# Kernel optimization log

Measured on AMD Instinct MI355X. Metric: run time of the kernel, lower is better.

The kernel has to match this reference:

```python
import jax, jax.numpy as jnp
import numpy as np

N, C, NS = 131072, 128, 16
BN_EPS = 1e-5


def setup_inputs() -> dict:
    key = jax.random.key(0)
    ks = jax.random.split(key, 8)
    p = jax.random.normal(ks[0], (N, 3), dtype=jnp.float32)
    u = jax.random.normal(ks[1], (N, C), dtype=jnp.float32)
    o = jnp.array([N], dtype=jnp.int32)  # batch offset (single cloud)
    idx = jax.random.randint(ks[2], (N, NS), 0, N, dtype=jnp.int32)  # precomputed KNN indices
    s = 1.0 / np.sqrt(C)
    W1 = jax.random.uniform(ks[3], (C, C), jnp.float32, -s, s)
    b1 = jax.random.uniform(ks[4], (C,), jnp.float32, -s, s)
    W2 = jax.random.uniform(ks[5], (C, C), jnp.float32, -s, s)
    b2 = jax.random.uniform(ks[6], (C,), jnp.float32, -s, s)
    gamma = jnp.ones((C,), jnp.float32)
    beta = jnp.zeros((C,), jnp.float32)
    return {"p": p, "u": u, "o": o, "idx": idx, "W1": W1, "b1": b1,
            "W2": W2, "b2": b2, "gamma": gamma, "beta": beta}


def reference(p, u, o, idx, W1, b1, W2, b2, gamma, beta):
    # pre_trans: Linear(d_in, d_in)
    u_pre = u @ W1 + b1                                  # [N, C]
    # queryandgroup (use_xyz=False): gather neighbor features by KNN idx
    u_n = u_pre[idx]                                     # [N, NS, C] irregular gather
    # local Laplacian: ReLU(neighbor - center), mean over neighborhood
    lap = jnp.maximum(u_n - u_pre[:, None, :], 0.0).mean(axis=1)  # [N, C]
    # varphi: Linear -> BatchNorm1d (training stats) -> ReLU
    h = lap @ W2 + b2                                    # [N, C]
    mean = h.mean(axis=0)
    var = ((h - mean) ** 2).mean(axis=0)  # biased var, as BN normalization uses
    h = (h - mean) * jax.lax.rsqrt(var + BN_EPS) * gamma + beta
    u_tt = jnp.maximum(h, 0.0)
    return (p, u_tt, o)
```

## Files before the change

### kernel.cpp

```cpp
#include <hip/hip_runtime.h>

#define N_PTS 131072
#define C_DIM 128
#define NS_K  16
#define BN_EPS 1e-5f

typedef unsigned short ushort_t;
typedef unsigned short u16x8 __attribute__((ext_vector_type(8)));
typedef __bf16 bf16x8 __attribute__((ext_vector_type(8)));
typedef float f32x4 __attribute__((ext_vector_type(4)));

__device__ __forceinline__ ushort_t f2b(float f) {
    unsigned int u = __float_as_uint(f);
    u += 0x7FFFu + ((u >> 16) & 1u);
    return (ushort_t)(u >> 16);
}
__device__ __forceinline__ float b2f(ushort_t h) {
    return __uint_as_float((unsigned int)h << 16);
}

__global__ __launch_bounds__(256) void prep_w_kernel(
    const float* __restrict__ W1, const float* __restrict__ W2,
    ushort_t* __restrict__ wT1, ushort_t* __restrict__ wT2)
{
    const int t = blockIdx.x * 256 + threadIdx.x;
    const int n = t & 127;
    const int k = t >> 7;
    wT1[n * 128 + k] = f2b(W1[k * 128 + n]);
    wT2[n * 128 + k] = f2b(W2[k * 128 + n]);
}

template <bool A_BF16, bool STATS>
__global__ __launch_bounds__(256) void gemm_mfma_kernel(
    const void* __restrict__ Aptr, const ushort_t* __restrict__ wT,
    const float* __restrict__ bias, ushort_t* __restrict__ out,
    float* __restrict__ gsum, float* __restrict__ gsq)
{
    __shared__ __align__(16) ushort_t a_sh[128 * 136];
    __shared__ __align__(16) ushort_t w_sh[128 * 136];
    __shared__ float s_sum[128];
    __shared__ float s_sq[128];

    const int tid  = threadIdx.x;
    const int lane = tid & 63;
    const int wv   = tid >> 6;
    const int m16  = lane & 15;
    const int q    = lane >> 4;
    const int base = blockIdx.x * 128;

    if (STATS && tid < 128) { s_sum[tid] = 0.f; s_sq[tid] = 0.f; }

    {
        const int row  = tid >> 1;
        const int half = (tid & 1) * 64;
        ushort_t* as = a_sh + row * 136 + half;
        if (A_BF16) {
            const ushort_t* ag = (const ushort_t*)Aptr + (size_t)(base + row) * 128 + half;
            #pragma unroll
            for (int j = 0; j < 8; j++)
                *(u16x8*)(as + j * 8) = *(const u16x8*)(ag + j * 8);
        } else {
            const float* ag = (const float*)Aptr + (size_t)(base + row) * 128 + half;
            #pragma unroll
            for (int j = 0; j < 8; j++) {
                f32x4 lo = *(const f32x4*)(ag + j * 8);
                f32x4 hi = *(const f32x4*)(ag + j * 8 + 4);
                u16x8 v;
                v[0] = f2b(lo[0]); v[1] = f2b(lo[1]); v[2] = f2b(lo[2]); v[3] = f2b(lo[3]);
                v[4] = f2b(hi[0]); v[5] = f2b(hi[1]); v[6] = f2b(hi[2]); v[7] = f2b(hi[3]);
                *(u16x8*)(as + j * 8) = v;
            }
        }
    }
    {
        const int n    = tid >> 1;
        const int half = (tid & 1) * 64;
        const ushort_t* wg = wT + (size_t)n * 128 + half;
        ushort_t* ws = w_sh + n * 136 + half;
        #pragma unroll
        for (int j = 0; j < 8; j++)
            *(u16x8*)(ws + j * 8) = *(const u16x8*)(wg + j * 8);
    }
    __syncthreads();

    f32x4 acc[2][8];
    #pragma unroll
    for (int i = 0; i < 2; i++)
        #pragma unroll
        for (int c = 0; c < 8; c++) acc[i][c] = (f32x4){0.f, 0.f, 0.f, 0.f};

    const ushort_t* ap0 = a_sh + ((wv * 2 + 0) * 16 + m16) * 136 + q * 8;
    const ushort_t* ap1 = a_sh + ((wv * 2 + 1) * 16 + m16) * 136 + q * 8;
    const ushort_t* wp  = w_sh + m16 * 136 + q * 8;

    #pragma unroll
    for (int k0 = 0; k0 < 128; k0 += 32) {
        bf16x8 a0 = __builtin_bit_cast(bf16x8, *(const u16x8*)(ap0 + k0));
        bf16x8 a1 = __builtin_bit_cast(bf16x8, *(const u16x8*)(ap1 + k0));
        #pragma unroll
        for (int c = 0; c < 8; c++) {
            bf16x8 b = __builtin_bit_cast(bf16x8, *(const u16x8*)(wp + c * (16 * 136) + k0));
            acc[0][c] = __builtin_amdgcn_mfma_f32_16x16x32_bf16(a0, b, acc[0][c], 0, 0, 0);
            acc[1][c] = __builtin_amdgcn_mfma_f32_16x16x32_bf16(a1, b, acc[1][c], 0, 0, 0);
        }
    }

    __syncthreads();

    float psum[8], psq[8];
    #pragma unroll
    for (int c = 0; c < 8; c++) { psum[c] = 0.f; psq[c] = 0.f; }

    #pragma unroll
    for (int c = 0; c < 8; c++) {
        const int col = c * 16 + m16;
        const float bv = bias[col];
        #pragma unroll
        for (int i = 0; i < 2; i++) {
            const int rb = (wv * 2 + i) * 16 + q * 4;
            #pragma unroll
            for (int r = 0; r < 4; r++) {
                const float v = acc[i][c][r] + bv;
                a_sh[(rb + r) * 136 + col] = f2b(v);
                if (STATS) { psum[c] += v; psq[c] += v * v; }
            }
        }
    }
    if (STATS) {
        #pragma unroll
        for (int c = 0; c < 8; c++) {
            atomicAdd(&s_sum[c * 16 + m16], psum[c]);
            atomicAdd(&s_sq[c * 16 + m16],  psq[c]);
        }
    }
    __syncthreads();

    {
        const int r0 = tid >> 4;
        const int c0 = (tid & 15) * 8;
        #pragma unroll
        for (int it = 0; it < 8; it++) {
            const int rl = r0 + it * 16;
            const u16x8 v = *(const u16x8*)(a_sh + rl * 136 + c0);
            *(u16x8*)(out + (size_t)(base + rl) * 128 + c0) = v;
        }
    }
    if (STATS && tid < 128) {
        atomicAdd(&gsum[tid], s_sum[tid]);
        atomicAdd(&gsq[tid],  s_sq[tid]);
    }
}

__global__ __launch_bounds__(256) void laplacian_kernel(
    const ushort_t* __restrict__ table, const int* __restrict__ idx,
    ushort_t* __restrict__ lap)
{
    __shared__ int s_idx[256];
    const int tid = threadIdx.x;
    s_idx[tid] = idx[blockIdx.x * 256 + tid];
    __syncthreads();

    const int p  = tid >> 4;
    const int c8 = (tid & 15) * 8;
    const size_t pt = (size_t)blockIdx.x * 16 + p;

    const u16x8 cv = *(const u16x8*)(table + pt * 128 + c8);
    float ctr[8];
    #pragma unroll
    for (int e = 0; e < 8; e++) ctr[e] = b2f(cv[e]);

    float acc[8];
    #pragma unroll
    for (int e = 0; e < 8; e++) acc[e] = 0.f;

    #pragma unroll
    for (int s = 0; s < NS_K; s++) {
        const int j = s_idx[p * 16 + s];
        const u16x8 nv = *(const u16x8*)(table + (size_t)j * 128 + c8);
        #pragma unroll
        for (int e = 0; e < 8; e++)
            acc[e] += fmaxf(b2f(nv[e]) - ctr[e], 0.f);
    }

    u16x8 o;
    #pragma unroll
    for (int e = 0; e < 8; e++) o[e] = f2b(acc[e] * (1.f / (float)NS_K));
    *(u16x8*)(lap + pt * 128 + c8) = o;
}

__global__ void bn_stats_kernel(const float* __restrict__ gsum,
                                const float* __restrict__ gsq,
                                const float* __restrict__ gamma,
                                const float* __restrict__ beta,
                                float* __restrict__ bnsc, float* __restrict__ bnsh)
{
    const int c = threadIdx.x;
    const float invN = 1.f / (float)N_PTS;
    const float mean = gsum[c] * invN;
    const float var  = gsq[c] * invN - mean * mean;
    const float sc   = rsqrtf(var + BN_EPS) * gamma[c];
    bnsc[c] = sc;
    bnsh[c] = fmaf(-mean, sc, beta[c]);
}

__global__ __launch_bounds__(256) void bn_relu_kernel(
    const ushort_t* __restrict__ h, const float* __restrict__ bnsc,
    const float* __restrict__ bnsh, float* __restrict__ out)
{
    const size_t i = (size_t)blockIdx.x * 256 + threadIdx.x;
    const int c8 = (threadIdx.x * 8) & 127;

    const u16x8 hv = *(const u16x8*)(h + i * 8);
    const f32x4 sc0 = *(const f32x4*)(bnsc + c8);
    const f32x4 sc1 = *(const f32x4*)(bnsc + c8 + 4);
    const f32x4 sh0 = *(const f32x4*)(bnsh + c8);
    const f32x4 sh1 = *(const f32x4*)(bnsh + c8 + 4);

    f32x4 o0, o1;
    #pragma unroll
    for (int e = 0; e < 4; e++) {
        o0[e] = fmaxf(fmaf(b2f(hv[e]),     sc0[e], sh0[e]), 0.f);
        o1[e] = fmaxf(fmaf(b2f(hv[4 + e]), sc1[e], sh1[e]), 0.f);
    }
    float* op = out + (size_t)3 * N_PTS + i * 8;
    *(f32x4*)(op)     = o0;
    *(f32x4*)(op + 4) = o1;
}

__global__ __launch_bounds__(256) void copy_p_kernel(
    const float* __restrict__ p, const int* __restrict__ o,
    float* __restrict__ out)
{
    const size_t i = (size_t)blockIdx.x * 256 + threadIdx.x;
    *(f32x4*)(out + i * 4) = *(const f32x4*)(p + i * 4);
    if (i == 0)
        out[(size_t)3 * N_PTS + (size_t)N_PTS * C_DIM] = (float)o[0];
}

extern "C" void kernel_launch(void* const* d_in, const int* in_sizes, int n_in,
                              void* d_out, int out_size, void* d_ws, size_t ws_size,
                              hipStream_t stream) {
    const float* p     = (const float*)d_in[0];
    const float* u     = (const float*)d_in[1];
    const int*   o     = (const int*)d_in[2];
    const int*   idx   = (const int*)d_in[3];
    const float* W1    = (const float*)d_in[4];
    const float* b1    = (const float*)d_in[5];
    const float* W2    = (const float*)d_in[6];
    const float* b2    = (const float*)d_in[7];
    const float* gamma = (const float*)d_in[8];
    const float* beta  = (const float*)d_in[9];
    float* out = (float*)d_out;

    char* ws = (char*)d_ws;
    const size_t buf_bytes = (size_t)N_PTS * C_DIM * sizeof(ushort_t);
    ushort_t* table = (ushort_t*)ws;
    ushort_t* lap   = (ushort_t*)(ws + buf_bytes);
    ushort_t* h     = (ushort_t*)(ws + 2 * buf_bytes);
    float*    stats = (float*)(ws + 3 * buf_bytes);
    float* gsum = stats;
    float* gsq  = stats + 128;
    float* bnsc = stats + 256;
    float* bnsh = stats + 384;
    ushort_t* wT1 = (ushort_t*)(stats + 512);
    ushort_t* wT2 = wT1 + 128 * 128;

    hipMemsetAsync(stats, 0, 256 * sizeof(float), stream);

    prep_w_kernel<<<64, 256, 0, stream>>>(W1, W2, wT1, wT2);
    gemm_mfma_kernel<false, false><<<N_PTS / 128, 256, 0, stream>>>(
        u, wT1, b1, table, nullptr, nullptr);
    laplacian_kernel<<<N_PTS / 16, 256, 0, stream>>>(table, idx, lap);
    gemm_mfma_kernel<true, true><<<N_PTS / 128, 256, 0, stream>>>(
        lap, wT2, b2, h, gsum, gsq);
    bn_stats_kernel<<<1, 128, 0, stream>>>(gsum, gsq, gamma, beta, bnsc, bnsh);
    bn_relu_kernel<<<(N_PTS * C_DIM / 8) / 256, 256, 0, stream>>>(
        h, bnsc, bnsh, out);
    copy_p_kernel<<<(3 * N_PTS / 4) / 256, 256, 0, stream>>>(p, o, out);
}
```

Baseline: 290.8 us.

## Fuse Laplacian gather into second GEMM and merge BN-ReLU with p copy

The Laplacian gather-mean is computed directly into shared memory inside the second MFMA GEMM kernel. This removes the intermediate lap buffer's global write and read and one kernel launch. The BN-ReLU and p-copy kernels are merged into one launch by splitting blocks by index. The fused kernel uses about 70KB of shared memory and an unroll-1 gather loop, which may lower occupancy and hide gather latency less well than the separate lightweight Laplacian kernel.

```diff
diff --git a/kernel.cpp b/kernel.cpp
--- a/kernel.cpp
+++ b/kernel.cpp
@@ -151,41 +151,138 @@
     }
 }
 
-__global__ __launch_bounds__(256) void laplacian_kernel(
+__global__ __launch_bounds__(256) void lap_gemm_kernel(
     const ushort_t* __restrict__ table, const int* __restrict__ idx,
-    ushort_t* __restrict__ lap)
-{
-    __shared__ int s_idx[256];
-    const int tid = threadIdx.x;
-    s_idx[tid] = idx[blockIdx.x * 256 + tid];
-    __syncthreads();
-
-    const int p  = tid >> 4;
-    const int c8 = (tid & 15) * 8;
-    const size_t pt = (size_t)blockIdx.x * 16 + p;
-
-    const u16x8 cv = *(const u16x8*)(table + pt * 128 + c8);
-    float ctr[8];
-    #pragma unroll
-    for (int e = 0; e < 8; e++) ctr[e] = b2f(cv[e]);
-
-    float acc[8];
-    #pragma unroll
-    for (int e = 0; e < 8; e++) acc[e] = 0.f;
-
-    #pragma unroll
-    for (int s = 0; s < NS_K; s++) {
-        const int j = s_idx[p * 16 + s];
-        const u16x8 nv = *(const u16x8*)(table + (size_t)j * 128 + c8);
-        #pragma unroll
-        for (int e = 0; e < 8; e++)
-            acc[e] += fmaxf(b2f(nv[e]) - ctr[e], 0.f);
-    }
-
-    u16x8 o;
-    #pragma unroll
-    for (int e = 0; e < 8; e++) o[e] = f2b(acc[e] * (1.f / (float)NS_K));
-    *(u16x8*)(lap + pt * 128 + c8) = o;
+    const ushort_t* __restrict__ wT, const float* __restrict__ bias,
+    ushort_t* __restrict__ out, float* __restrict__ gsum, float* __restrict__ gsq)
+{
+    __shared__ __align__(16) ushort_t a_sh[128 * 136];
+    __shared__ __align__(16) ushort_t w_sh[128 * 136];
+    __shared__ __align__(16) int s_idx[128 * NS_K];
+    __shared__ float s_sum[128];
+    __shared__ float s_sq[128];
+
+    const int tid  = threadIdx.x;
+    const int lane = tid & 63;
+    const int wv   = tid >> 6;
+    const int m16  = lane & 15;
+    const int q    = lane >> 4;
+    const int base = blockIdx.x * 128;
+
+    if (tid < 128) { s_sum[tid] = 0.f; s_sq[tid] = 0.f; }
+
+    {
+        const int4* ig = (const int4*)(idx + (size_t)base * NS_K);
+        int4* is = (int4*)s_idx;
+        is[tid]       = ig[tid];
+        is[tid + 256] = ig[tid + 256];
+    }
+    {
+        const int n    = tid >> 1;
+        const int half = (tid & 1) * 64;
+        const ushort_t* wg = wT + (size_t)n * 128 + half;
+        ushort_t* ws = w_sh + n * 136 + half;
+        #pragma unroll
+        for (int j = 0; j < 8; j++)
+            *(u16x8*)(ws + j * 8) = *(const u16x8*)(wg + j * 8);
+    }
+    __syncthreads();
+
+    {
+        const int pl = tid >> 4;
+        const int c8 = (tid & 15) * 8;
+        #pragma unroll 1
+        for (int it = 0; it < 8; it++) {
+            const int pp = it * 16 + pl;
+            const u16x8 cv = *(const u16x8*)(table + (size_t)(base + pp) * 128 + c8);
+            float ctr[8];
+            #pragma unroll
+            for (int e = 0; e < 8; e++) ctr[e] = b2f(cv[e]);
+
+            float lacc[8];
+            #pragma unroll
+            for (int e = 0; e < 8; e++) lacc[e] = 0.f;
+
+            #pragma unroll
+            for (int s = 0; s < NS_K; s++) {
+                const int j = s_idx[pp * NS_K + s];
+                const u16x8 nv = *(const u16x8*)(table + (size_t)j * 128 + c8);
+                #pragma unroll
+                for (int e = 0; e < 8; e++)
+                    lacc[e] += fmaxf(b2f(nv[e]) - ctr[e], 0.f);
+            }
+            u16x8 ov;
+            #pragma unroll
+            for (int e = 0; e < 8; e++) ov[e] = f2b(lacc[e] * (1.f / (float)NS_K));
+            *(u16x8*)(a_sh + pp * 136 + c8) = ov;
+        }
+    }
+    __syncthreads();
+
+    f32x4 acc[2][8];
+    #pragma unroll
+    for (int i = 0; i < 2; i++)
+        #pragma unroll
+        for (int c = 0; c < 8; c++) acc[i][c] = (f32x4){0.f, 0.f, 0.f, 0.f};
+
+    const ushort_t* ap0 = a_sh + ((wv * 2 + 0) * 16 + m16) * 136 + q * 8;
+    const ushort_t* ap1 = a_sh + ((wv * 2 + 1) * 16 + m16) * 136 + q * 8;
+    const ushort_t* wp  = w_sh + m16 * 136 + q * 8;
+
+    #pragma unroll
+    for (int k0 = 0; k0 < 128; k0 += 32) {
+        bf16x8 a0 = __builtin_bit_cast(bf16x8, *(const u16x8*)(ap0 + k0));
+        bf16x8 a1 = __builtin_bit_cast(bf16x8, *(const u16x8*)(ap1 + k0));
+        #pragma unroll
+        for (int c = 0; c < 8; c++) {
+            bf16x8 b = __builtin_bit_cast(bf16x8, *(const u16x8*)(wp + c * (16 * 136) + k0));
+            acc[0][c] = __builtin_amdgcn_mfma_f32_16x16x32_bf16(a0, b, acc[0][c], 0, 0, 0);
+            acc[1][c] = __builtin_amdgcn_mfma_f32_16x16x32_bf16(a1, b, acc[1][c], 0, 0, 0);
+        }
+    }
+
+    __syncthreads();
+
+    float psum[8], psq[8];
+    #pragma unroll
+    for (int c = 0; c < 8; c++) { psum[c] = 0.f; psq[c] = 0.f; }
+
+    #pragma unroll
+    for (int c = 0; c < 8; c++) {
+        const int col = c * 16 + m16;
+        const float bv = bias[col];
+        #pragma unroll
+        for (int i = 0; i < 2; i++) {
+            const int rb = (wv * 2 + i) * 16 + q * 4;
+            #pragma unroll
+            for (int r = 0; r < 4; r++) {
+                const float v = acc[i][c][r] + bv;
+                a_sh[(rb + r) * 136 + col] = f2b(v);
+                psum[c] += v; psq[c] += v * v;
+            }
+        }
+    }
+    #pragma unroll
+    for (int c = 0; c < 8; c++) {
+        atomicAdd(&s_sum[c * 16 + m16], psum[c]);
+        atomicAdd(&s_sq[c * 16 + m16],  psq[c]);
+    }
+    __syncthreads();
+
+    {
+        const int r0 = tid >> 4;
+        const int c0 = (tid & 15) * 8;
+        #pragma unroll
+        for (int it = 0; it < 8; it++) {
+            const int rl = r0 + it * 16;
+            const u16x8 v = *(const u16x8*)(a_sh + rl * 136 + c0);
+            *(u16x8*)(out + (size_t)(base + rl) * 128 + c0) = v;
+        }
+    }
+    if (tid < 128) {
+        atomicAdd(&gsum[tid], s_sum[tid]);
+        atomicAdd(&gsq[tid],  s_sq[tid]);
+    }
 }
 
 __global__ void bn_stats_kernel(const float* __restrict__ gsum,
@@ -203,38 +300,40 @@
     bnsh[c] = fmaf(-mean, sc, beta[c]);
 }
 
-__global__ __launch_bounds__(256) void bn_relu_kernel(
+#define BN_BLOCKS ((N_PTS * C_DIM / 8) / 256)
+#define P_BLOCKS  ((3 * N_PTS / 4) / 256)
+
+__global__ __launch_bounds__(256) void bn_relu_p_kernel(
     const ushort_t* __restrict__ h, const float* __restrict__ bnsc,
-    const float* __restrict__ bnsh, float* __restrict__ out)
-{
-    const size_t i = (size_t)blockIdx.x * 256 + threadIdx.x;
-    const int c8 = (threadIdx.x * 8) & 127;
-
-    const u16x8 hv = *(const u16x8*)(h + i * 8);
-    const f32x4 sc0 = *(const f32x4*)(bnsc + c8);
-    const f32x4 sc1 = *(const f32x4*)(bnsc + c8 + 4);
-    const f32x4 sh0 = *(const f32x4*)(bnsh + c8);
-    const f32x4 sh1 = *(const f32x4*)(bnsh + c8 + 4);
-
-    f32x4 o0, o1;
-    #pragma unroll
-    for (int e = 0; e < 4; e++) {
-        o0[e] = fmaxf(fmaf(b2f(hv[e]),     sc0[e], sh0[e]), 0.f);
-        o1[e] = fmaxf(fmaf(b2f(hv[4 + e]), sc1[e], sh1[e]), 0.f);
-    }
-    float* op = out + (size_t)3 * N_PTS + i * 8;
-    *(f32x4*)(op)     = o0;
-    *(f32x4*)(op + 4) = o1;
-}
-
-__global__ __launch_bounds__(256) void copy_p_kernel(
-    const float* __restrict__ p, const int* __restrict__ o,
-    float* __restrict__ out)
-{
-    const size_t i = (size_t)blockIdx.x * 256 + threadIdx.x;
-    *(f32x4*)(out + i * 4) = *(const f32x4*)(p + i * 4);
-    if (i == 0)
-        out[(size_t)3 * N_PTS + (size_t)N_PTS * C_DIM] = (float)o[0];
+    const float* __restrict__ bnsh, const float* __restrict__ p,
+    const int* __restrict__ o, float* __restrict__ out)
+{
+    const int b = blockIdx.x;
+    if (b < BN_BLOCKS) {
+        const size_t i = (size_t)b * 256 + threadIdx.x;
+        const int c8 = (threadIdx.x * 8) & 127;
+
+        const u16x8 hv = *(const u16x8*)(h + i * 8);
+        const f32x4 sc0 = *(const f32x4*)(bnsc + c8);
+        const f32x4 sc1 = *(const f32x4*)(bnsc + c8 + 4);
+        const f32x4 sh0 = *(const f32x4*)(bnsh + c8);
+        const f32x4 sh1 = *(const f32x4*)(bnsh + c8 + 4);
+
+        f32x4 o0, o1;
+        #pragma unroll
+        for (int e = 0; e < 4; e++) {
+            o0[e] = fmaxf(fmaf(b2f(hv[e]),     sc0[e], sh0[e]), 0.f);
+            o1[e] = fmaxf(fmaf(b2f(hv[4 + e]), sc1[e], sh1[e]), 0.f);
+        }
+        float* op = out + (size_t)3 * N_PTS + i * 8;
+        *(f32x4*)(op)     = o0;
+        *(f32x4*)(op + 4) = o1;
+    } else {
+        const size_t i = (size_t)(b - BN_BLOCKS) * 256 + threadIdx.x;
+        *(f32x4*)(out + i * 4) = *(const f32x4*)(p + i * 4);
+        if (i == 0)
+            out[(size_t)3 * N_PTS + (size_t)N_PTS * C_DIM] = (float)o[0];
+    }
 }
 
 extern "C" void kernel_launch(void* const* d_in, const int* in_sizes, int n_in,
@@ -255,9 +354,8 @@
     char* ws = (char*)d_ws;
     const size_t buf_bytes = (size_t)N_PTS * C_DIM * sizeof(ushort_t);
     ushort_t* table = (ushort_t*)ws;
-    ushort_t* lap   = (ushort_t*)(ws + buf_bytes);
-    ushort_t* h     = (ushort_t*)(ws + 2 * buf_bytes);
-    float*    stats = (float*)(ws + 3 * buf_bytes);
+    ushort_t* h     = (ushort_t*)(ws + buf_bytes);
+    float*    stats = (float*)(ws + 2 * buf_bytes);
     float* gsum = stats;
     float* gsq  = stats + 128;
     float* bnsc = stats + 256;
@@ -270,11 +368,9 @@
     prep_w_kernel<<<64, 256, 0, stream>>>(W1, W2, wT1, wT2);
     gemm_mfma_kernel<false, false><<<N_PTS / 128, 256, 0, stream>>>(
         u, wT1, b1, table, nullptr, nullptr);
-    laplacian_kernel<<<N_PTS / 16, 256, 0, stream>>>(table, idx, lap);
-    gemm_mfma_kernel<true, true><<<N_PTS / 128, 256, 0, stream>>>(
-        lap, wT2, b2, h, gsum, gsq);
+    lap_gemm_kernel<<<N_PTS / 128, 256, 0, stream>>>(
+        table, idx, wT2, b2, h, gsum, gsq);
     bn_stats_kernel<<<1, 128, 0, stream>>>(gsum, gsq, gamma, beta, bnsc, bnsh);
-    bn_relu_kernel<<<(N_PTS * C_DIM / 8) / 256, 256, 0, stream>>>(
-        h, bnsc, bnsh, out);
-    copy_p_kernel<<<(3 * N_PTS / 4) / 256, 256, 0, stream>>>(p, o, out);
-}
+    bn_relu_p_kernel<<<BN_BLOCKS + P_BLOCKS, 256, 0, stream>>>(
+        h, bnsc, bnsh, p, o, out);
+}
```

After: 286.6 us. Within noise of the previous version (-1.4%).
